# Performance work log

Hardware: AMD Instinct MI355X
Metric: run time of the kernel (lower is better)

Reference implementation:

```python
import jax, jax.numpy as jnp
import numpy as np

B, IN, D = 4096, 2048, 2048
NAMES = ["inpgate", "rec_inpgate", "mem_inpgate", "inp", "rec_inp", "readgate",
         "rec_readgate", "mem_readgate", "decoder", "writegate", "rec_writegate",
         "mem_writegate", "encoder"]


def setup_inputs() -> dict:
    key = jax.random.key(0)
    ks = jax.random.split(key, 1 + len(NAMES))
    inp = {
        "x": jax.random.normal(ks[0], (B, IN), jnp.float32),
        "out0": jnp.zeros((B, D), jnp.float32),   # recurrent output state (reset())
        "mem0": jnp.zeros((B, D), jnp.float32),   # memory state (reset())
    }
    for i, n in enumerate(NAMES):
        inp["w_" + n] = jax.random.normal(ks[1 + i], (D, D), jnp.float32) * 0.02
        inp["b_" + n] = jnp.zeros((D,), jnp.float32)
    return inp


def _lin(v, W, b):
    # torch nn.Linear: y = v @ W.T + b, W is [out, in]
    return v @ W.T + b


def reference(x, out0, mem0,
              w_inpgate, b_inpgate, w_rec_inpgate, b_rec_inpgate,
              w_mem_inpgate, b_mem_inpgate, w_inp, b_inp,
              w_rec_inp, b_rec_inp, w_readgate, b_readgate,
              w_rec_readgate, b_rec_readgate, w_mem_readgate, b_mem_readgate,
              w_decoder, b_decoder, w_writegate, b_writegate,
              w_rec_writegate, b_rec_writegate, w_mem_writegate, b_mem_writegate,
              w_encoder, b_encoder):
    sig = jax.nn.sigmoid
    # input block (note: original uses sigmoid here, not tanh)
    block_inp = sig(_lin(x, w_inp, b_inp) + _lin(out0, w_rec_inp, b_rec_inp))
    inp_gate = sig(_lin(x, w_inpgate, b_inpgate)
                   + _lin(mem0, w_mem_inpgate, b_mem_inpgate)
                   + _lin(out0, w_rec_inpgate, b_rec_inpgate))
    read_gate = sig(_lin(x, w_readgate, b_readgate)
                    + _lin(mem0, w_mem_readgate, b_mem_readgate)
                    + _lin(out0, w_rec_readgate, b_rec_readgate))
    decoded_mem = _lin(read_gate * mem0, w_decoder, b_decoder)
    hidden = decoded_mem + block_inp * inp_gate
    write_gate = sig(_lin(x, w_writegate, b_writegate)
                     + _lin(mem0, w_mem_writegate, b_mem_writegate)
                     + _lin(out0, w_rec_writegate, b_rec_writegate))
    enc = jnp.tanh(_lin(hidden, w_encoder, b_encoder))
    mem = (1.0 - write_gate) * mem0 + write_gate * enc
    # torch forward() returns self.out (== hidden_act); mem is internal state
    return hidden
```

## Files before the change

kernel.cpp:

```cpp
#include <hip/hip_runtime.h>
#include <stdint.h>


typedef short bf16x8 __attribute__((ext_vector_type(8)));
typedef float f32x4 __attribute__((ext_vector_type(4)));

#define AS1(p) ((__attribute__((address_space(1))) void*)(uintptr_t)(p))
#define AS3(p) ((__attribute__((address_space(3))) void*)(uint32_t)(uintptr_t)(p))
#define GLD16(gp, lp) __builtin_amdgcn_global_load_lds(AS1(gp), AS3(lp), 16, 0, 0)

template <bool B> struct BoolC { static constexpr bool value = B; };

__device__ __forceinline__ unsigned short f2bf(float f) {
  union { float f; unsigned u; } c; c.f = f;
  unsigned u = c.u;
  unsigned r = (u + 0x7FFFu + ((u >> 16) & 1u)) >> 16;
  return (unsigned short)r;
}
__device__ __forceinline__ float bf2f(unsigned short h) {
  union { unsigned u; float f; } c; c.u = ((unsigned)h) << 16;
  return c.f;
}
__device__ __forceinline__ float sigf(float x) {
  return 1.0f / (1.0f + __expf(-x));
}

__global__ void init_flags_kernel(int* flags) {
  if (threadIdx.x < 2) flags[threadIdx.x] = 0;
}

struct ConvActArgs {
  const float4* src[3];
  ushort4* dst[3];
  int flagidx[3];
  int n4;
  int* flags;
};

__global__ void conv_acts_kernel(ConvActArgs a) {
  const int arr = blockIdx.y;
  const float4* __restrict__ s = a.src[arr];
  ushort4* __restrict__ d = a.dst[arr];
  unsigned nz = 0;
  for (int i = blockIdx.x * blockDim.x + threadIdx.x; i < a.n4;
       i += gridDim.x * blockDim.x) {
    float4 v = s[i];
    union { float f; unsigned u; } cx, cy, cz, cw;
    cx.f = v.x; cy.f = v.y; cz.f = v.z; cw.f = v.w;
    nz |= cx.u | cy.u | cz.u | cw.u;
    ushort4 o;
    o.x = f2bf(v.x); o.y = f2bf(v.y); o.z = f2bf(v.z); o.w = f2bf(v.w);
    d[i] = o;
  }
  const int fi = a.flagidx[arr];
  if (fi >= 0) {
    if (__any(nz != 0u) && (threadIdx.x & 63) == 0) atomicOr(&a.flags[fi], 1);
  }
}

struct ConvWArgs {
  const float4* src[9];
  ushort4* dst[9];
  int flagidx[9];
  int n4;
  const int* flags;
};

__global__ void conv_weights_kernel(ConvWArgs a) {
  const int arr = blockIdx.y;
  const int fi = a.flagidx[arr];
  if (fi >= 0 && a.flags[fi] == 0) return;
  const float4* __restrict__ s = a.src[arr];
  ushort4* __restrict__ d = a.dst[arr];
  for (int i = blockIdx.x * blockDim.x + threadIdx.x; i < a.n4;
       i += gridDim.x * blockDim.x) {
    float4 v = s[i];
    ushort4 o;
    o.x = f2bf(v.x); o.y = f2bf(v.y); o.z = f2bf(v.z); o.w = f2bf(v.w);
    d[i] = o;
  }
}

struct DualArgs {
  const unsigned short *xb, *o0b, *m0b;
  const unsigned short *Winp, *Wrecinp, *Winpgate, *Wrecinpgate, *Wmeminpgate;
  const float *b_inp, *b_rec_inp, *b_inpgate, *b_rec_inpgate, *b_mem_inpgate;
  const float* b_dec;
  const int* flags;
  unsigned short *u1, *u2;
  float* outF;
};

__global__ void __launch_bounds__(512, 2)
gemm_dual(DualArgs a) {
  __shared__ __attribute__((aligned(16))) unsigned short sA[2][256 * 64];
  __shared__ __attribute__((aligned(16))) unsigned short sB1[2][128 * 64];
  __shared__ __attribute__((aligned(16))) unsigned short sB2[2][128 * 64];

  const int tid = threadIdx.x;
  const int l = tid & 63;
  const int w = tid >> 6;
  const int wm = w >> 2, wn = w & 3;
  const int bm = blockIdx.y, bn = blockIdx.x;

  f32x4 acc1[8][2], acc2[8][2];
#pragma unroll
  for (int i = 0; i < 8; ++i)
#pragma unroll
    for (int j = 0; j < 2; ++j) {
      acc1[i][j] = (f32x4){0.f, 0.f, 0.f, 0.f};
      acc2[i][j] = (f32x4){0.f, 0.f, 0.f, 0.f};
    }

  const int srow = l >> 3;
  const int kchS = (l & 7) ^ srow;
  const long long laneA = ((long long)(bm * 256) + srow) * 2048 + kchS * 8;
  const long long laneB = ((long long)(bn * 128) + srow) * 2048 + kchS * 8;

  const int rB = w * 16;
  const int rA0 = (w & 3) * 16 + (w >> 2) * 128;

  auto run_pass = [&](auto dc, const unsigned short* Ap,
                      const unsigned short* W1p, const unsigned short* W2p) {
    constexpr bool DUAL = decltype(dc)::value;
    const unsigned short* ga = Ap + laneA;
    const unsigned short* g1 = DUAL ? (W1p + laneB) : (const unsigned short*)0;
    const unsigned short* g2 = W2p + laneB;

    if constexpr (DUAL) {
      GLD16(g1 + (long long)rB * 2048,       (char*)sB1[0] + rB * 128);
      GLD16(g1 + (long long)(rB + 8) * 2048, (char*)sB1[0] + (rB + 8) * 128);
    }
    GLD16(g2 + (long long)rB * 2048,         (char*)sB2[0] + rB * 128);
    GLD16(g2 + (long long)(rB + 8) * 2048,   (char*)sB2[0] + (rB + 8) * 128);
    GLD16(ga + (long long)rA0 * 2048,        (char*)sA[0] + rA0 * 128);
    GLD16(ga + (long long)(rA0 + 8) * 2048,  (char*)sA[0] + (rA0 + 8) * 128);
    GLD16(ga + (long long)(rA0 + 64) * 2048, (char*)sA[0] + (rA0 + 64) * 128);
    GLD16(ga + (long long)(rA0 + 72) * 2048, (char*)sA[0] + (rA0 + 72) * 128);
    asm volatile("s_waitcnt vmcnt(2)" ::: "memory");
    __builtin_amdgcn_s_barrier();

    for (int kt = 0; kt < 31; ++kt) {
      const int cur = kt & 1, nxt = cur ^ 1;
      const unsigned short* gan = ga + 64;
      const unsigned short* g1n = g1 + (DUAL ? 64 : 0);
      const unsigned short* g2n = g2 + 64;
#pragma unroll
      for (int p = 0; p < 4; ++p) {
        const int ks = p >> 1, ih = p & 1;
        bf16x8 af[4], b1f[2], b2f[2];
        const int c = ks * 4 + (l >> 4);
#pragma unroll
        for (int i = 0; i < 4; ++i) {
          const int ra = wm * 128 + ih * 64 + i * 16 + (l & 15);
          af[i] = *(const bf16x8*)((const char*)sA[cur] +
                                   (ra * 128 + ((c ^ (ra & 7)) * 16)));
        }
#pragma unroll
        for (int j = 0; j < 2; ++j) {
          const int rb = wn * 32 + j * 16 + (l & 15);
          if constexpr (DUAL)
            b1f[j] = *(const bf16x8*)((const char*)sB1[cur] +
                                      (rb * 128 + ((c ^ (rb & 7)) * 16)));
          b2f[j] = *(const bf16x8*)((const char*)sB2[cur] +
                                    (rb * 128 + ((c ^ (rb & 7)) * 16)));
        }
        if constexpr (DUAL) {
          if (p == 0) {
            GLD16(g1n + (long long)rB * 2048,       (char*)sB1[nxt] + rB * 128);
            GLD16(g1n + (long long)(rB + 8) * 2048, (char*)sB1[nxt] + (rB + 8) * 128);
          } else if (p == 1) {
            GLD16(g2n + (long long)rB * 2048,       (char*)sB2[nxt] + rB * 128);
            GLD16(g2n + (long long)(rB + 8) * 2048, (char*)sB2[nxt] + (rB + 8) * 128);
          } else if (p == 2) {
            GLD16(gan + (long long)rA0 * 2048,       (char*)sA[nxt] + rA0 * 128);
            GLD16(gan + (long long)(rA0 + 8) * 2048, (char*)sA[nxt] + (rA0 + 8) * 128);
          } else {
            GLD16(gan + (long long)(rA0 + 64) * 2048, (char*)sA[nxt] + (rA0 + 64) * 128);
            GLD16(gan + (long long)(rA0 + 72) * 2048, (char*)sA[nxt] + (rA0 + 72) * 128);
          }
        } else {
          if (p == 0) {
            GLD16(g2n + (long long)rB * 2048,       (char*)sB2[nxt] + rB * 128);
            GLD16(g2n + (long long)(rB + 8) * 2048, (char*)sB2[nxt] + (rB + 8) * 128);
          } else if (p == 1) {
            GLD16(gan + (long long)rA0 * 2048,       (char*)sA[nxt] + rA0 * 128);
            GLD16(gan + (long long)(rA0 + 8) * 2048, (char*)sA[nxt] + (rA0 + 8) * 128);
          } else if (p == 2) {
            GLD16(gan + (long long)(rA0 + 64) * 2048, (char*)sA[nxt] + (rA0 + 64) * 128);
            GLD16(gan + (long long)(rA0 + 72) * 2048, (char*)sA[nxt] + (rA0 + 72) * 128);
          }
        }
        __builtin_amdgcn_s_barrier();
        asm volatile("s_waitcnt lgkmcnt(0)" ::: "memory");
        __builtin_amdgcn_s_setprio(1);
#pragma unroll
        for (int i = 0; i < 4; ++i)
#pragma unroll
          for (int j = 0; j < 2; ++j) {
            if constexpr (DUAL)
              acc1[ih * 4 + i][j] = __builtin_amdgcn_mfma_f32_16x16x32_bf16(
                  af[i], b1f[j], acc1[ih * 4 + i][j], 0, 0, 0);
            acc2[ih * 4 + i][j] = __builtin_amdgcn_mfma_f32_16x16x32_bf16(
                af[i], b2f[j], acc2[ih * 4 + i][j], 0, 0, 0);
          }
        __builtin_amdgcn_s_setprio(0);
        if (p == 0 || p == 3)
          asm volatile("s_waitcnt vmcnt(2)" ::: "memory");
        __builtin_amdgcn_s_barrier();
      }
      ga += 64;
      if constexpr (DUAL) g1 += 64;
      g2 += 64;
    }

    {
      const int cur = 1;
#pragma unroll
      for (int p = 0; p < 4; ++p) {
        const int ks = p >> 1, ih = p & 1;
        bf16x8 af[4], b1f[2], b2f[2];
        const int c = ks * 4 + (l >> 4);
#pragma unroll
        for (int i = 0; i < 4; ++i) {
          const int ra = wm * 128 + ih * 64 + i * 16 + (l & 15);
          af[i] = *(const bf16x8*)((const char*)sA[cur] +
                                   (ra * 128 + ((c ^ (ra & 7)) * 16)));
        }
#pragma unroll
        for (int j = 0; j < 2; ++j) {
          const int rb = wn * 32 + j * 16 + (l & 15);
          if constexpr (DUAL)
            b1f[j] = *(const bf16x8*)((const char*)sB1[cur] +
                                      (rb * 128 + ((c ^ (rb & 7)) * 16)));
          b2f[j] = *(const bf16x8*)((const char*)sB2[cur] +
                                    (rb * 128 + ((c ^ (rb & 7)) * 16)));
        }
        __builtin_amdgcn_s_barrier();
        asm volatile("s_waitcnt lgkmcnt(0)" ::: "memory");
        __builtin_amdgcn_s_setprio(1);
#pragma unroll
        for (int i = 0; i < 4; ++i)
#pragma unroll
          for (int j = 0; j < 2; ++j) {
            if constexpr (DUAL)
              acc1[ih * 4 + i][j] = __builtin_amdgcn_mfma_f32_16x16x32_bf16(
                  af[i], b1f[j], acc1[ih * 4 + i][j], 0, 0, 0);
            acc2[ih * 4 + i][j] = __builtin_amdgcn_mfma_f32_16x16x32_bf16(
                af[i], b2f[j], acc2[ih * 4 + i][j], 0, 0, 0);
          }
        __builtin_amdgcn_s_setprio(0);
        if (p == 0)
          asm volatile("s_waitcnt vmcnt(0)" ::: "memory");
        __builtin_amdgcn_s_barrier();
      }
    }
  };

  const int f_out0 = a.flags[0];
  const int f_mem0 = a.flags[1];

  run_pass(BoolC<true>{}, a.xb, a.Winp, a.Winpgate);
  if (f_out0) run_pass(BoolC<true>{}, a.o0b, a.Wrecinp, a.Wrecinpgate);
  if (f_mem0) run_pass(BoolC<false>{}, a.m0b, (const unsigned short*)0, a.Wmeminpgate);

  const int colb = bn * 128 + wn * 32;
  const int rowb = bm * 256 + wm * 128;
  const bool fast = (f_mem0 == 0);
#pragma unroll
  for (int j = 0; j < 2; ++j) {
    const int col = colb + j * 16 + (l & 15);
    const float s1 = a.b_inp[col] + a.b_rec_inp[col];
    const float s2 = a.b_inpgate[col] + a.b_rec_inpgate[col] + a.b_mem_inpgate[col];
    const float bd = fast ? a.b_dec[col] : 0.f;
#pragma unroll
    for (int ii = 0; ii < 8; ++ii) {
      const int row0 = rowb + (ii >> 2) * 64 + (ii & 3) * 16 + (l >> 4) * 4;
#pragma unroll
      for (int r = 0; r < 4; ++r) {
        const long long idx = (long long)(row0 + r) * 2048 + col;
        const float u1v = acc1[ii][j][r] + s1;
        const float u2v = acc2[ii][j][r] + s2;
        if (fast) {
          a.outF[idx] = sigf(u1v) * sigf(u2v) + bd;
        } else {
          a.u1[idx] = f2bf(u1v);
          a.u2[idx] = f2bf(u2v);
        }
      }
    }
  }
}

struct Job {
  const unsigned short* A0; const unsigned short* W0; const float* b0;
  const unsigned short* A1; const unsigned short* W1; const float* b1;
  const unsigned short* A2; const unsigned short* W2; const float* b2;
  int f0, f1, f2;
  int npairs;
  int jobf;
  const int* flags;
  const float* add;
  float* outF;
  unsigned short* outH;
};

__global__ void __launch_bounds__(256)
gemm_bt_multi(Job jb) {
  __shared__ __attribute__((aligned(16))) unsigned short sA[128 * 64];
  __shared__ __attribute__((aligned(16))) unsigned short sB[128 * 64];

  if (jb.jobf >= 0 && jb.flags[jb.jobf] == 0) return;

  const int tid = threadIdx.x;
  const int l = tid & 63;
  const int w = tid >> 6;
  const int wm = w >> 1, wn = w & 1;
  const int bm = blockIdx.y, bn = blockIdx.x;

  f32x4 acc[4][4];
#pragma unroll
  for (int i = 0; i < 4; ++i)
#pragma unroll
    for (int j = 0; j < 4; ++j) acc[i][j] = (f32x4){0.f, 0.f, 0.f, 0.f};

  const int srow = l >> 3;
  const int kchS = (l & 7) ^ srow;
  const long long laneA = ((long long)bm * 128 + srow) * 2048 + kchS * 8;
  const long long laneB = ((long long)bn * 128 + srow) * 2048 + kchS * 8;

  auto do_pair = [&](const unsigned short* Ap, const unsigned short* Wp) {
    const unsigned short* ga = Ap + laneA;
    const unsigned short* gb = Wp + laneB;
    for (int kt = 0; kt < 32; ++kt) {
#pragma unroll
      for (int ii = 0; ii < 4; ++ii) {
        const int q = w * 4 + ii;
        GLD16(ga + (long long)(q * 8) * 2048, (char*)sA + q * 1024);
        GLD16(gb + (long long)(q * 8) * 2048, (char*)sB + q * 1024);
      }
      __syncthreads();
#pragma unroll
      for (int ks = 0; ks < 2; ++ks) {
        bf16x8 af[4], bf[4];
        const int c = ks * 4 + (l >> 4);
#pragma unroll
        for (int i = 0; i < 4; ++i) {
          const int ra = wm * 64 + i * 16 + (l & 15);
          const int rb = wn * 64 + i * 16 + (l & 15);
          af[i] = *(const bf16x8*)((const char*)sA + (ra * 128 + ((c ^ (ra & 7)) * 16)));
          bf[i] = *(const bf16x8*)((const char*)sB + (rb * 128 + ((c ^ (rb & 7)) * 16)));
        }
#pragma unroll
        for (int i = 0; i < 4; ++i)
#pragma unroll
          for (int j = 0; j < 4; ++j)
            acc[i][j] = __builtin_amdgcn_mfma_f32_16x16x32_bf16(
                af[i], bf[j], acc[i][j], 0, 0, 0);
      }
      __syncthreads();
      ga += 64;
      gb += 64;
    }
  };

  if (jb.f0 < 0 || jb.flags[jb.f0]) do_pair(jb.A0, jb.W0);
  if (jb.npairs > 1 && (jb.f1 < 0 || jb.flags[jb.f1])) do_pair(jb.A1, jb.W1);
  if (jb.npairs > 2 && (jb.f2 < 0 || jb.flags[jb.f2])) do_pair(jb.A2, jb.W2);

  const int colb = bn * 128 + wn * 64;
  const int rowb = bm * 128 + wm * 64;
#pragma unroll
  for (int j = 0; j < 4; ++j) {
    const int col = colb + j * 16 + (l & 15);
    float bias = 0.f;
    if (jb.b0) bias += jb.b0[col];
    if (jb.npairs > 1 && jb.b1) bias += jb.b1[col];
    if (jb.npairs > 2 && jb.b2) bias += jb.b2[col];
#pragma unroll
    for (int i = 0; i < 4; ++i) {
      const int row0 = rowb + i * 16 + (l >> 4) * 4;
#pragma unroll
      for (int r = 0; r < 4; ++r) {
        const long long idx = (long long)(row0 + r) * 2048 + col;
        float v = acc[i][j][r] + bias;
        if (jb.add) v += jb.add[idx];
        if (jb.outF) jb.outF[idx] = v;
        else jb.outH[idx] = f2bf(v);
      }
    }
  }
}

__global__ void gates_kernel(const ushort4* __restrict__ u1,
                             const ushort4* __restrict__ u2,
                             const ushort4* __restrict__ u3,
                             const float4* __restrict__ mem0,
                             float4* __restrict__ g, ushort4* __restrict__ rg,
                             const int* flags, int n4) {
  if (flags[1] == 0) return;
  int i = blockIdx.x * blockDim.x + threadIdx.x;
  if (i >= n4) return;
  ushort4 a = u1[i], b = u2[i], c = u3[i];
  float4 m = mem0[i];
  float4 go;
  ushort4 ro;
  go.x = sigf(bf2f(a.x)) * sigf(bf2f(b.x)); ro.x = f2bf(sigf(bf2f(c.x)) * m.x);
  go.y = sigf(bf2f(a.y)) * sigf(bf2f(b.y)); ro.y = f2bf(sigf(bf2f(c.y)) * m.y);
  go.z = sigf(bf2f(a.z)) * sigf(bf2f(b.z)); ro.z = f2bf(sigf(bf2f(c.z)) * m.z);
  go.w = sigf(bf2f(a.w)) * sigf(bf2f(b.w)); ro.w = f2bf(sigf(bf2f(c.w)) * m.w);
  g[i] = go;
  rg[i] = ro;
}

extern "C" void kernel_launch(void* const* d_in, const int* in_sizes, int n_in,
                              void* d_out, int out_size, void* d_ws, size_t ws_size,
                              hipStream_t stream) {
  (void)in_sizes; (void)n_in; (void)out_size; (void)ws_size;
  const int Bx = 4096, Dx = 2048;
  const size_t ACT = (size_t)Bx * Dx;
  const size_t WEL = (size_t)Dx * Dx;

  const float* x    = (const float*)d_in[0];
  const float* out0 = (const float*)d_in[1];
  const float* mem0 = (const float*)d_in[2];
  const float* w_inpgate     = (const float*)d_in[3];
  const float* b_inpgate     = (const float*)d_in[4];
  const float* w_rec_inpgate = (const float*)d_in[5];
  const float* b_rec_inpgate = (const float*)d_in[6];
  const float* w_mem_inpgate = (const float*)d_in[7];
  const float* b_mem_inpgate = (const float*)d_in[8];
  const float* w_inp         = (const float*)d_in[9];
  const float* b_inp         = (const float*)d_in[10];
  const float* w_rec_inp     = (const float*)d_in[11];
  const float* b_rec_inp     = (const float*)d_in[12];
  const float* w_readgate    = (const float*)d_in[13];
  const float* b_readgate    = (const float*)d_in[14];
  const float* w_rec_readgate= (const float*)d_in[15];
  const float* b_rec_readgate= (const float*)d_in[16];
  const float* w_mem_readgate= (const float*)d_in[17];
  const float* b_mem_readgate= (const float*)d_in[18];
  const float* w_decoder     = (const float*)d_in[19];
  const float* b_decoder     = (const float*)d_in[20];

  char* ws = (char*)d_ws;
  unsigned short* xb  = (unsigned short*)(ws);
  unsigned short* o0b = xb + ACT;
  unsigned short* m0b = o0b + ACT;
  unsigned short* wb  = m0b + ACT;
  unsigned short* u1 = wb + 9 * WEL;
  unsigned short* u2 = u1 + ACT;
  unsigned short* u3 = u2 + ACT;
  float* g = (float*)(u3 + ACT);
  unsigned short* rg = (unsigned short*)(g + ACT);
  int* flags = (int*)(rg + ACT);

  init_flags_kernel<<<1, 64, 0, stream>>>(flags);

  ConvActArgs aa;
  aa.src[0] = (const float4*)x;    aa.dst[0] = (ushort4*)xb;  aa.flagidx[0] = -1;
  aa.src[1] = (const float4*)out0; aa.dst[1] = (ushort4*)o0b; aa.flagidx[1] = 0;
  aa.src[2] = (const float4*)mem0; aa.dst[2] = (ushort4*)m0b; aa.flagidx[2] = 1;
  aa.n4 = (int)(ACT / 4);
  aa.flags = flags;
  conv_acts_kernel<<<dim3(2048, 3, 1), 256, 0, stream>>>(aa);

  ConvWArgs wa;
  const float* wsrc[9] = {w_inp, w_rec_inp, w_inpgate, w_mem_inpgate,
                          w_rec_inpgate, w_readgate, w_mem_readgate,
                          w_rec_readgate, w_decoder};
  const int wflag[9] = {-1, 0, -1, 1, 0, 1, 1, 0, 1};
  for (int i = 0; i < 9; ++i) {
    wa.src[i] = (const float4*)wsrc[i];
    wa.dst[i] = (ushort4*)(wb + (size_t)i * WEL);
    wa.flagidx[i] = wflag[i];
  }
  wa.n4 = (int)(WEL / 4);
  wa.flags = flags;
  conv_weights_kernel<<<dim3(1024, 9, 1), 256, 0, stream>>>(wa);

  DualArgs da;
  da.xb = xb; da.o0b = o0b; da.m0b = m0b;
  da.Winp = wb + 0 * WEL;      da.Wrecinp = wb + 1 * WEL;
  da.Winpgate = wb + 2 * WEL;  da.Wrecinpgate = wb + 4 * WEL;
  da.Wmeminpgate = wb + 3 * WEL;
  da.b_inp = b_inp; da.b_rec_inp = b_rec_inp;
  da.b_inpgate = b_inpgate; da.b_rec_inpgate = b_rec_inpgate;
  da.b_mem_inpgate = b_mem_inpgate;
  da.b_dec = b_decoder;
  da.flags = flags;
  da.u1 = u1; da.u2 = u2;
  da.outF = (float*)d_out;
  gemm_dual<<<dim3(16, 16, 1), 512, 0, stream>>>(da);

  Job J2 = {};
  J2.A0 = xb;  J2.W0 = wb + 5 * WEL; J2.b0 = b_readgate;      J2.f0 = -1;
  J2.A1 = m0b; J2.W1 = wb + 6 * WEL; J2.b1 = b_mem_readgate;  J2.f1 = 1;
  J2.A2 = o0b; J2.W2 = wb + 7 * WEL; J2.b2 = b_rec_readgate;  J2.f2 = 0;
  J2.npairs = 3; J2.jobf = 1; J2.flags = flags; J2.outH = u3;
  gemm_bt_multi<<<dim3(16, 32, 1), 256, 0, stream>>>(J2);

  gates_kernel<<<(int)(ACT / 4 + 255) / 256, 256, 0, stream>>>(
      (const ushort4*)u1, (const ushort4*)u2, (const ushort4*)u3,
      (const float4*)mem0, (float4*)g, (ushort4*)rg, flags, (int)(ACT / 4));

  Job JD = {};
  JD.A0 = rg; JD.W0 = wb + 8 * WEL; JD.b0 = b_decoder; JD.f0 = 1;
  JD.npairs = 1; JD.jobf = 1; JD.flags = flags;
  JD.add = g; JD.outF = (float*)d_out;
  gemm_bt_multi<<<dim3(16, 32, 1), 256, 0, stream>>>(JD);
}
```

Baseline: 370.3 us.

## Restructure GEMM main loop into stage-then-compute with two barriers per k-tile

Replaces the four-phase interleaved prefetch schedule, which had per-phase barriers and a setprio hint, with a simpler loop. Each k-tile issues the whole next-tile global->LDS load up front, waits on vmcnt for the current tile, then runs all MFMAs for both k-substeps between only two barriers. The staging layout changes to contiguous 8-row groups per wave. This cuts barrier count per tile from eight to two, at the risk of less interleaving between loads and MFMAs and higher register pressure from holding eight A fragments.

Measured after the change: 369.2 us. About the same (-0.3%).

```diff
diff --git a/kernel.cpp b/kernel.cpp
--- a/kernel.cpp
+++ b/kernel.cpp
@@ -117,9 +117,6 @@
   const long long laneA = ((long long)(bm * 256) + srow) * 2048 + kchS * 8;
   const long long laneB = ((long long)(bn * 128) + srow) * 2048 + kchS * 8;
 
-  const int rB = w * 16;
-  const int rA0 = (w & 3) * 16 + (w >> 2) * 128;
-
   auto run_pass = [&](auto dc, const unsigned short* Ap,
                       const unsigned short* W1p, const unsigned short* W2p) {
     constexpr bool DUAL = decltype(dc)::value;
@@ -127,134 +124,80 @@
     const unsigned short* g1 = DUAL ? (W1p + laneB) : (const unsigned short*)0;
     const unsigned short* g2 = W2p + laneB;
 
-    if constexpr (DUAL) {
-      GLD16(g1 + (long long)rB * 2048,       (char*)sB1[0] + rB * 128);
-      GLD16(g1 + (long long)(rB + 8) * 2048, (char*)sB1[0] + (rB + 8) * 128);
-    }
-    GLD16(g2 + (long long)rB * 2048,         (char*)sB2[0] + rB * 128);
-    GLD16(g2 + (long long)(rB + 8) * 2048,   (char*)sB2[0] + (rB + 8) * 128);
-    GLD16(ga + (long long)rA0 * 2048,        (char*)sA[0] + rA0 * 128);
-    GLD16(ga + (long long)(rA0 + 8) * 2048,  (char*)sA[0] + (rA0 + 8) * 128);
-    GLD16(ga + (long long)(rA0 + 64) * 2048, (char*)sA[0] + (rA0 + 64) * 128);
-    GLD16(ga + (long long)(rA0 + 72) * 2048, (char*)sA[0] + (rA0 + 72) * 128);
-    asm volatile("s_waitcnt vmcnt(2)" ::: "memory");
-    __builtin_amdgcn_s_barrier();
-
-    for (int kt = 0; kt < 31; ++kt) {
-      const int cur = kt & 1, nxt = cur ^ 1;
-      const unsigned short* gan = ga + 64;
-      const unsigned short* g1n = g1 + (DUAL ? 64 : 0);
-      const unsigned short* g2n = g2 + 64;
-#pragma unroll
-      for (int p = 0; p < 4; ++p) {
-        const int ks = p >> 1, ih = p & 1;
-        bf16x8 af[4], b1f[2], b2f[2];
+    auto stage = [&](int buf, long long koff) {
+#pragma unroll
+      for (int ii = 0; ii < 4; ++ii) {
+        const int q = w * 4 + ii;
+        GLD16(ga + koff + (long long)(q * 8) * 2048, (char*)sA[buf] + q * 1024);
+      }
+#pragma unroll
+      for (int ii = 0; ii < 2; ++ii) {
+        const int q = w * 2 + ii;
+        if constexpr (DUAL)
+          GLD16(g1 + koff + (long long)(q * 8) * 2048, (char*)sB1[buf] + q * 1024);
+        GLD16(g2 + koff + (long long)(q * 8) * 2048, (char*)sB2[buf] + q * 1024);
+      }
+    };
+
+    auto compute = [&](int buf) {
+#pragma unroll
+      for (int ks = 0; ks < 2; ++ks) {
+        bf16x8 af[8], b1f[2], b2f[2];
         const int c = ks * 4 + (l >> 4);
 #pragma unroll
-        for (int i = 0; i < 4; ++i) {
-          const int ra = wm * 128 + ih * 64 + i * 16 + (l & 15);
-          af[i] = *(const bf16x8*)((const char*)sA[cur] +
-                                   (ra * 128 + ((c ^ (ra & 7)) * 16)));
-        }
+        for (int ih = 0; ih < 2; ++ih)
+#pragma unroll
+          for (int i = 0; i < 4; ++i) {
+            const int ra = wm * 128 + ih * 64 + i * 16 + (l & 15);
+            af[ih * 4 + i] = *(const bf16x8*)(
+                (const char*)sA[buf] + (ra * 128 + ((c ^ (ra & 7)) * 16)));
+          }
 #pragma unroll
         for (int j = 0; j < 2; ++j) {
           const int rb = wn * 32 + j * 16 + (l & 15);
           if constexpr (DUAL)
-            b1f[j] = *(const bf16x8*)((const char*)sB1[cur] +
-                                      (rb * 128 + ((c ^ (rb & 7)) * 16)));
-          b2f[j] = *(const bf16x8*)((const char*)sB2[cur] +
-                                    (rb * 128 + ((c ^ (rb & 7)) * 16)));
+            b1f[j] = *(const bf16x8*)(
+                (const char*)sB1[buf] + (rb * 128 + ((c ^ (rb & 7)) * 16)));
+          b2f[j] = *(const bf16x8*)(
+              (const char*)sB2[buf] + (rb * 128 + ((c ^ (rb & 7)) * 16)));
         }
-        if constexpr (DUAL) {
-          if (p == 0) {
-            GLD16(g1n + (long long)rB * 2048,       (char*)sB1[nxt] + rB * 128);
-            GLD16(g1n + (long long)(rB + 8) * 2048, (char*)sB1[nxt] + (rB + 8) * 128);
-          } else if (p == 1) {
-            GLD16(g2n + (long long)rB * 2048,       (char*)sB2[nxt] + rB * 128);
-            GLD16(g2n + (long long)(rB + 8) * 2048, (char*)sB2[nxt] + (rB + 8) * 128);
-          } else if (p == 2) {
-            GLD16(gan + (long long)rA0 * 2048,       (char*)sA[nxt] + rA0 * 128);
-            GLD16(gan + (long long)(rA0 + 8) * 2048, (char*)sA[nxt] + (rA0 + 8) * 128);
-          } else {
-            GLD16(gan + (long long)(rA0 + 64) * 2048, (char*)sA[nxt] + (rA0 + 64) * 128);
-            GLD16(gan + (long long)(rA0 + 72) * 2048, (char*)sA[nxt] + (rA0 + 72) * 128);
-          }
-        } else {
-          if (p == 0) {
-            GLD16(g2n + (long long)rB * 2048,       (char*)sB2[nxt] + rB * 128);
-            GLD16(g2n + (long long)(rB + 8) * 2048, (char*)sB2[nxt] + (rB + 8) * 128);
-          } else if (p == 1) {
-            GLD16(gan + (long long)rA0 * 2048,       (char*)sA[nxt] + rA0 * 128);
-            GLD16(gan + (long long)(rA0 + 8) * 2048, (char*)sA[nxt] + (rA0 + 8) * 128);
-          } else if (p == 2) {
-            GLD16(gan + (long long)(rA0 + 64) * 2048, (char*)sA[nxt] + (rA0 + 64) * 128);
-            GLD16(gan + (long long)(rA0 + 72) * 2048, (char*)sA[nxt] + (rA0 + 72) * 128);
-          }
-        }
-        __builtin_amdgcn_s_barrier();
-        asm volatile("s_waitcnt lgkmcnt(0)" ::: "memory");
-        __builtin_amdgcn_s_setprio(1);
-#pragma unroll
-        for (int i = 0; i < 4; ++i)
-#pragma unroll
-          for (int j = 0; j < 2; ++j) {
-            if constexpr (DUAL)
-              acc1[ih * 4 + i][j] = __builtin_amdgcn_mfma_f32_16x16x32_bf16(
-                  af[i], b1f[j], acc1[ih * 4 + i][j], 0, 0, 0);
-            acc2[ih * 4 + i][j] = __builtin_amdgcn_mfma_f32_16x16x32_bf16(
-                af[i], b2f[j], acc2[ih * 4 + i][j], 0, 0, 0);
-          }
-        __builtin_amdgcn_s_setprio(0);
-        if (p == 0 || p == 3)
-          asm volatile("s_waitcnt vmcnt(2)" ::: "memory");
-        __builtin_amdgcn_s_barrier();
-      }
-      ga += 64;
-      if constexpr (DUAL) g1 += 64;
-      g2 += 64;
+#pragma unroll
+        for (int ih = 0; ih < 2; ++ih)
+#pragma unroll
+          for (int i = 0; i < 4; ++i)
+#pragma unroll
+            for (int j = 0; j < 2; ++j) {
+              if constexpr (DUAL)
+                acc1[ih * 4 + i][j] = __builtin_amdgcn_mfma_f32_16x16x32_bf16(
+                    af[ih * 4 + i], b1f[j], acc1[ih * 4 + i][j], 0, 0, 0);
+              acc2[ih * 4 + i][j] = __builtin_amdgcn_mfma_f32_16x16x32_bf16(
+                  af[ih * 4 + i], b2f[j], acc2[ih * 4 + i][j], 0, 0, 0);
+            }
+      }
+    };
+
+    stage(0, 0);
+
+    for (int kt = 0; kt < 31; ++kt) {
+      const int cur = kt & 1;
+      stage(cur ^ 1, (long long)(kt + 1) * 64);
+      if constexpr (DUAL)
+        asm volatile("s_waitcnt vmcnt(8)" ::: "memory");
+      else
+        asm volatile("s_waitcnt vmcnt(6)" ::: "memory");
+      __builtin_amdgcn_s_barrier();
+      asm volatile("" ::: "memory");
+      compute(cur);
+      asm volatile("s_waitcnt lgkmcnt(0)" ::: "memory");
+      __builtin_amdgcn_s_barrier();
     }
 
-    {
-      const int cur = 1;
-#pragma unroll
-      for (int p = 0; p < 4; ++p) {
-        const int ks = p >> 1, ih = p & 1;
-        bf16x8 af[4], b1f[2], b2f[2];
-        const int c = ks * 4 + (l >> 4);
-#pragma unroll
-        for (int i = 0; i < 4; ++i) {
-          const int ra = wm * 128 + ih * 64 + i * 16 + (l & 15);
-          af[i] = *(const bf16x8*)((const char*)sA[cur] +
-                                   (ra * 128 + ((c ^ (ra & 7)) * 16)));
-        }
-#pragma unroll
-        for (int j = 0; j < 2; ++j) {
-          const int rb = wn * 32 + j * 16 + (l & 15);
-          if constexpr (DUAL)
-            b1f[j] = *(const bf16x8*)((const char*)sB1[cur] +
-                                      (rb * 128 + ((c ^ (rb & 7)) * 16)));
-          b2f[j] = *(const bf16x8*)((const char*)sB2[cur] +
-                                    (rb * 128 + ((c ^ (rb & 7)) * 16)));
-        }
-        __builtin_amdgcn_s_barrier();
-        asm volatile("s_waitcnt lgkmcnt(0)" ::: "memory");
-        __builtin_amdgcn_s_setprio(1);
-#pragma unroll
-        for (int i = 0; i < 4; ++i)
-#pragma unroll
-          for (int j = 0; j < 2; ++j) {
-            if constexpr (DUAL)
-              acc1[ih * 4 + i][j] = __builtin_amdgcn_mfma_f32_16x16x32_bf16(
-                  af[i], b1f[j], acc1[ih * 4 + i][j], 0, 0, 0);
-            acc2[ih * 4 + i][j] = __builtin_amdgcn_mfma_f32_16x16x32_bf16(
-                af[i], b2f[j], acc2[ih * 4 + i][j], 0, 0, 0);
-          }
-        __builtin_amdgcn_s_setprio(0);
-        if (p == 0)
-          asm volatile("s_waitcnt vmcnt(0)" ::: "memory");
-        __builtin_amdgcn_s_barrier();
-      }
-    }
+    asm volatile("s_waitcnt vmcnt(0)" ::: "memory");
+    __builtin_amdgcn_s_barrier();
+    asm volatile("" ::: "memory");
+    compute(1);
+    asm volatile("s_waitcnt lgkmcnt(0)" ::: "memory");
+    __builtin_amdgcn_s_barrier();
   };
 
   const int f_out0 = a.flags[0];
```
